# Optimization experiments

Hardware: AMD Instinct MI355X
Metric: run time of the kernel (lower is better)

The kernel has to match this reference:

```python
import jax, jax.numpy as jnp
import numpy as np

L_DEG = 4      # max out-degree L
DEPTH = 7      # complete L-ary tree depth -> 21845 nodes
N_GEN = 16
C_ST = 8
M_LAB = 256


def _build_tree():
    sizes = [L_DEG ** d for d in range(DEPTH + 1)]
    limits = np.concatenate([[0], np.cumsum(sizes)]).astype(np.int64)
    t_size = int(limits[-1])
    nodes = np.arange(t_size)
    rng = np.random.default_rng(0)
    labels = rng.integers(0, M_LAB, t_size)
    parent = np.where(nodes > 0, (nodes - 1) // L_DEG, 0)
    pos = np.where(nodes > 0, (nodes - 1) % L_DEG, 0)
    ch = np.zeros((t_size, L_DEG), dtype=np.int64)
    n_internal = int(limits[-2])
    ch[:n_internal] = L_DEG * nodes[:n_internal, None] + np.arange(1, L_DEG + 1)[None, :]
    t = np.concatenate([labels[:, None], parent[:, None], pos[:, None], ch], axis=1).astype(np.int64)
    return t, limits


def setup_inputs() -> dict:
    key = jax.random.key(0)
    ka, kb, kp, ks = jax.random.split(key, 4)
    t, limits = _build_tree()
    return {
        "t": jnp.asarray(t),
        "t_limits": jnp.asarray(limits),
        "a": jax.random.normal(ka, (N_GEN, C_ST, C_ST, L_DEG), dtype=jnp.float32),
        "b": jax.random.normal(kb, (N_GEN, C_ST, M_LAB), dtype=jnp.float32),
        "pi": jax.random.normal(kp, (N_GEN, C_ST, L_DEG), dtype=jnp.float32),
        "sp": jax.random.normal(ks, (N_GEN, L_DEG), dtype=jnp.float32),
    }


def _forward(tn, lim, a, b, pi, sp):
    # tn, lim are host numpy int arrays (tree structure is a constant).
    G, C, _, L = a.shape
    t_size = int(lim[-1])
    n_levels = len(lim) - 1
    sL = int(lim[-2])                      # first leaf index
    labels = tn[:, 0]
    posf = tn[:, 2]
    ch_all = tn[:, 3:3 + L]

    sm_a = jax.nn.softmax(a, axis=1)       # P(parent_state i | child_state j, pos l)
    sm_b = jax.nn.softmax(b, axis=2)
    sm_pi = jax.nn.softmax(pi, axis=1)
    sm_sp = jax.nn.softmax(sp, axis=1)
    a_sp = sm_a * sm_sp[:, None, None, :]  # [G,i,j,L]

    # ---------------- upward pass ----------------
    prior = jnp.zeros((t_size, G, C), a.dtype)
    beta = jnp.zeros((t_size, G, C), a.dtype)
    beta_il = jnp.zeros((t_size, G, C), a.dtype)

    prior_lv = jnp.moveaxis(sm_pi[:, :, posf[sL:]], 2, 0)   # [NL,G,C]
    emis_lv = jnp.moveaxis(sm_b[:, :, labels[sL:]], 2, 0)   # [NL,G,C]
    beta_lv = prior_lv * emis_lv
    beta_lv = beta_lv / jnp.sum(beta_lv, axis=2, keepdims=True)
    prior = prior.at[sL:].set(prior_lv)
    beta = beta.at[sL:].set(beta_lv)

    for lev in range(n_levels - 2, -1, -1):   # internal levels, bottom-up
        s, e = int(lim[lev]), int(lim[lev + 1])
        ch = ch_all[s:e]                       # [P,L]
        mask = (ch > 0).astype(a.dtype)        # children packed in first slots
        prior_ch = prior[ch]                   # [P,L,G,C]
        beta_ch = beta[ch]                     # [P,L,G,C]
        u_prior = jnp.einsum('gijl,pl,plgj->pgi', a_sp, mask, prior_ch)
        u_bil = jnp.einsum('gijl,pl,plgj->pgi', a_sp, mask, beta_ch) / u_prior
        emis = jnp.moveaxis(sm_b[:, :, labels[s:e]], 2, 0)  # [P,G,C]
        tmp = emis * u_bil * u_prior
        u_beta = tmp / jnp.sum(tmp, axis=2, keepdims=True)
        prior = prior.at[s:e].set(u_prior)
        beta = beta.at[s:e].set(u_beta)
        beta_il = beta_il.at[s:e].set(u_bil)

    # ---------------- downward pass ----------------
    # row t_size is a dummy slot for padded (absent) children
    eps_i = jnp.zeros((t_size + 1, G, C), a.dtype).at[0].set(beta[0])
    eps_ijl = jnp.zeros((t_size, G, C, C, L), a.dtype)
    for lev in range(0, n_levels - 1):         # parents, top-down (root included)
        s, e = int(lim[lev]), int(lim[lev + 1])
        ch = ch_all[s:e]
        maskb = ch > 0
        mask = maskb.astype(a.dtype)
        beta_ch = jnp.transpose(beta[ch], (0, 2, 3, 1))       # [P,G,Cj,L]
        pe = eps_i[s:e] / (prior[s:e] * beta_il[s:e])         # [P,G,Ci]
        res = (pe[:, :, :, None, None] * a_sp[None]
               * beta_ch[:, :, None, :, :]
               * mask[:, None, None, None, :])                # [P,G,i,j,L]
        child_eps = jnp.sum(res, axis=3)                       # sum over j (as in source) -> [P,G,i,L]
        vals = jnp.moveaxis(child_eps, 3, 1).reshape(-1, G, C) # [P*L,G,C]
        safe = np.where(maskb, ch, t_size).reshape(-1)
        eps_i = eps_i.at[safe].set(vals)
        eps_ijl = eps_ijl.at[s:e].set(res)
    eps_i = eps_i[:t_size]
    # leaves' eps_ijl stay zero (source scatters zeros there)

    # ---------------- log-likelihood ----------------
    a_lh = jnp.einsum('ugijl,gijl->g', eps_ijl, jnp.log(sm_a))
    b_lh = jnp.einsum('ugc,gcu->g', eps_i, jnp.log(sm_b)[:, :, labels])
    pi_lh = jnp.einsum('ugc,gcu->g', eps_i[sL:], jnp.log(sm_pi)[:, :, posf[sL:]])
    eps_l = jnp.sum(eps_ijl, axis=(2, 3))                      # [u,g,L]
    sp_lh = jnp.einsum('ugl,gl->g', eps_l, jnp.log(sm_sp))
    return a_lh + b_lh + pi_lh + sp_lh


def reference(t, t_limits, a, b, pi, sp):
    tn = np.asarray(t)
    lim = np.asarray(t_limits)
    return _forward(tn, lim, a, b, pi, sp)
```

## Files before the change

### kernel.cpp

```cpp
#include <hip/hip_runtime.h>


#define G 16
#define C 8
#define GC 128
#define TSIZE 21845
#define SL 5461

__device__ __forceinline__ float grp8_sum(float v) {
  v += __shfl_xor(v, 1);
  v += __shfl_xor(v, 2);
  v += __shfl_xor(v, 4);
  return v;
}

__global__ void setup_kernel(const float* __restrict__ ain, const float* __restrict__ bin,
                             const float* __restrict__ piin, const float* __restrict__ spin,
                             float* __restrict__ a_sp, float* __restrict__ log_a,
                             float* __restrict__ sm_bT, float* __restrict__ log_bT,
                             float* __restrict__ sm_piT, float* __restrict__ log_piT,
                             float* __restrict__ log_sp, float* __restrict__ out) {
  int blk = blockIdx.x, tid = threadIdx.x;
  if (blk < 16) {
    int g = blk;
    __shared__ float red4[4];
    for (int c = 0; c < 8; ++c) {
      int row = g * 8 + c;
      float x = bin[row * 256 + tid];
      float m = x;
      #pragma unroll
      for (int off2 = 32; off2; off2 >>= 1) m = fmaxf(m, __shfl_xor(m, off2));
      if ((tid & 63) == 0) red4[tid >> 6] = m;
      __syncthreads();
      m = fmaxf(fmaxf(red4[0], red4[1]), fmaxf(red4[2], red4[3]));
      __syncthreads();
      float e = expf(x - m);
      float ssum = e;
      #pragma unroll
      for (int off2 = 32; off2; off2 >>= 1) ssum += __shfl_xor(ssum, off2);
      if ((tid & 63) == 0) red4[tid >> 6] = ssum;
      __syncthreads();
      ssum = red4[0] + red4[1] + red4[2] + red4[3];
      __syncthreads();
      sm_bT[tid * GC + row]  = e / ssum;
      log_bT[tid * GC + row] = (x - m) - logf(ssum);
    }
  } else if (blk == 16) {
    for (int col = tid; col < 512; col += 256) {
      int g = col >> 5, j = (col >> 2) & 7, l = col & 3;
      float x[8], m = -1e30f;
      #pragma unroll
      for (int i = 0; i < 8; ++i) { x[i] = ain[g*256 + i*32 + j*4 + l]; m = fmaxf(m, x[i]); }
      float ssum = 0.f;
      #pragma unroll
      for (int i = 0; i < 8; ++i) ssum += expf(x[i] - m);
      float ls = logf(ssum);
      float y0 = spin[g*4+0], y1 = spin[g*4+1], y2 = spin[g*4+2], y3 = spin[g*4+3];
      float ms = fmaxf(fmaxf(y0, y1), fmaxf(y2, y3));
      float d = expf(y0-ms) + expf(y1-ms) + expf(y2-ms) + expf(y3-ms);
      float spv = expf(spin[g*4+l] - ms) / d;
      #pragma unroll
      for (int i = 0; i < 8; ++i) {
        int o2 = g*256 + i*32 + j*4 + l;
        float smv = expf(x[i] - m) / ssum;
        a_sp[o2]  = smv * spv;
        log_a[o2] = (x[i] - m) - ls;
      }
    }
  } else {
    if (tid < 64) {
      int g = tid >> 2, l = tid & 3;
      float x[8], m = -1e30f;
      #pragma unroll
      for (int c = 0; c < 8; ++c) { x[c] = piin[g*32 + c*4 + l]; m = fmaxf(m, x[c]); }
      float ssum = 0.f;
      #pragma unroll
      for (int c = 0; c < 8; ++c) ssum += expf(x[c] - m);
      float ls = logf(ssum);
      #pragma unroll
      for (int c = 0; c < 8; ++c) {
        sm_piT[l*GC + g*8 + c]  = expf(x[c] - m) / ssum;
        log_piT[l*GC + g*8 + c] = (x[c] - m) - ls;
      }
    } else if (tid < 80) {
      int g = tid - 64;
      float y[4], m = -1e30f;
      #pragma unroll
      for (int l = 0; l < 4; ++l) { y[l] = spin[g*4 + l]; m = fmaxf(m, y[l]); }
      float ssum = 0.f;
      #pragma unroll
      for (int l = 0; l < 4; ++l) ssum += expf(y[l] - m);
      float ls = logf(ssum);
      #pragma unroll
      for (int l = 0; l < 4; ++l) log_sp[g*4 + l] = (y[l] - m) - ls;
    } else if (tid >= 128 && tid < 144) {
      out[tid - 128] = 0.0f;
    }
  }
}

__device__ __forceinline__ void up_step(int u, int gi, const float* asp,
    const float* __restrict__ sm_bT, const int* __restrict__ t,
    float* __restrict__ beta, float* __restrict__ numbeta) {
  int ch0 = 4*u + 1;
  int g8 = gi & 0x78;
  float ub = 0.f;
  #pragma unroll
  for (int l = 0; l < 4; ++l) {
    const float4* bp = (const float4*)(beta + (size_t)(ch0 + l) * GC + g8);
    float4 b0 = bp[0], b1 = bp[1];
    ub += asp[l]*b0.x + asp[4+l]*b0.y + asp[8+l]*b0.z + asp[12+l]*b0.w
        + asp[16+l]*b1.x + asp[20+l]*b1.y + asp[24+l]*b1.z + asp[28+l]*b1.w;
  }
  float tmp = sm_bT[t[u*7] * GC + gi] * ub;
  float s = grp8_sum(tmp);
  size_t o = (size_t)u * GC + gi;
  beta[o]    = tmp / s;
  numbeta[o] = ub;
}

__device__ __forceinline__ double down_step(int u, int gi, const float* asp,
    const float* aal, const float* lsp,
    const float* __restrict__ log_bT, const int* __restrict__ t,
    const float* __restrict__ numbeta, const float* __restrict__ beta,
    float* __restrict__ eps) {
  size_t o = (size_t)u * GC + gi;
  float e  = eps[o];
  float pe = e / numbeta[o];
  int ch0 = 4*u + 1;
  int g8 = gi & 0x78;
  float local = 0.f;
  #pragma unroll
  for (int l = 0; l < 4; ++l) {
    const float4* bp = (const float4*)(beta + (size_t)(ch0 + l) * GC + g8);
    float4 b0 = bp[0], b1 = bp[1];
    float S = asp[l]*b0.x + asp[4+l]*b0.y + asp[8+l]*b0.z + asp[12+l]*b0.w
            + asp[16+l]*b1.x + asp[20+l]*b1.y + asp[24+l]*b1.z + asp[28+l]*b1.w;
    float A = aal[l]*b0.x + aal[4+l]*b0.y + aal[8+l]*b0.z + aal[12+l]*b0.w
            + aal[16+l]*b1.x + aal[20+l]*b1.y + aal[24+l]*b1.z + aal[28+l]*b1.w;
    float ce = pe * S;
    eps[(size_t)(ch0 + l) * GC + gi] = ce;
    local += pe*A + ce*lsp[l];
  }
  return (double)local + (double)(e * log_bT[t[u*7] * GC + gi]);
}

__global__ __launch_bounds__(512, 2) void up_kernel(
    const float* __restrict__ a_sp, const float* __restrict__ sm_bT,
    const float* __restrict__ sm_piT, const int* __restrict__ t,
    float* __restrict__ beta, float* __restrict__ numbeta) {
  int b = blockIdx.x, tid = threadIdx.x;
  int gi = tid & 127;
  float asp[32];
  {
    const float4* pa = (const float4*)(a_sp + (gi >> 3)*256 + (gi & 7)*32);
    #pragma unroll
    for (int q = 0; q < 8; ++q) {
      float4 v = pa[q];
      asp[q*4+0]=v.x; asp[q*4+1]=v.y; asp[q*4+2]=v.z; asp[q*4+3]=v.w;
    }
  }
  for (int it = 0; it < 16; ++it) {
    int k = it*4 + (tid >> 7);
    int u = SL + b*64 + k;
    float bt = sm_piT[(k & 3) * GC + gi] * sm_bT[t[u*7] * GC + gi];
    float s = grp8_sum(bt);
    beta[(size_t)u * GC + gi] = bt / s;
  }
  __syncthreads();
  for (int it = 0; it < 4; ++it)
    up_step(1365 + b*16 + it*4 + (tid >> 7), gi, asp, sm_bT, t, beta, numbeta);
  __syncthreads();
  up_step(341 + b*4 + (tid >> 7), gi, asp, sm_bT, t, beta, numbeta);
  __syncthreads();
  if (tid < 128) up_step(85 + b, gi, asp, sm_bT, t, beta, numbeta);
}

__global__ __launch_bounds__(512, 2) void top_kernel(
    const float* __restrict__ a_sp, const float* __restrict__ log_a,
    const float* __restrict__ log_sp, const float* __restrict__ sm_bT,
    const float* __restrict__ log_bT, const int* __restrict__ t,
    float* __restrict__ beta, float* __restrict__ numbeta,
    float* __restrict__ eps, float* __restrict__ out) {
  int g = blockIdx.x, tid = threadIdx.x;
  int i = tid & 7, gi = g*8 + i, q = tid >> 3;
  float asp[32], aal[32], lsp[4];
  {
    const float4* pa = (const float4*)(a_sp + g*256 + i*32);
    const float4* pl = (const float4*)(log_a + g*256 + i*32);
    #pragma unroll
    for (int k = 0; k < 8; ++k) {
      float4 va = pa[k], vl = pl[k];
      asp[k*4+0]=va.x; asp[k*4+1]=va.y; asp[k*4+2]=va.z; asp[k*4+3]=va.w;
      aal[k*4+0]=va.x*vl.x; aal[k*4+1]=va.y*vl.y; aal[k*4+2]=va.z*vl.z; aal[k*4+3]=va.w*vl.w;
    }
    #pragma unroll
    for (int l = 0; l < 4; ++l) lsp[l] = log_sp[g*4 + l];
  }
  up_step(21 + q, gi, asp, sm_bT, t, beta, numbeta);
  __syncthreads();
  if (tid < 128) up_step(5 + q, gi, asp, sm_bT, t, beta, numbeta);
  __syncthreads();
  if (tid < 32)  up_step(1 + q, gi, asp, sm_bT, t, beta, numbeta);
  __syncthreads();
  if (tid < 8) {
    up_step(0, gi, asp, sm_bT, t, beta, numbeta);
    eps[gi] = beta[gi];
  }
  __syncthreads();
  double acc = 0.0;
  if (tid < 8)   acc += down_step(0, gi, asp, aal, lsp, log_bT, t, numbeta, beta, eps);
  __syncthreads();
  if (tid < 32)  acc += down_step(1 + q, gi, asp, aal, lsp, log_bT, t, numbeta, beta, eps);
  __syncthreads();
  if (tid < 128) acc += down_step(5 + q, gi, asp, aal, lsp, log_bT, t, numbeta, beta, eps);
  __syncthreads();
  acc += down_step(21 + q, gi, asp, aal, lsp, log_bT, t, numbeta, beta, eps);
  acc += __shfl_xor(acc, 1);
  acc += __shfl_xor(acc, 2);
  acc += __shfl_xor(acc, 4);
  __shared__ double sd[64];
  if (i == 0) sd[tid >> 3] = acc;
  __syncthreads();
  if (tid == 0) {
    double s = 0.0;
    for (int k = 0; k < 64; ++k) s += sd[k];
    atomicAdd(&out[g], (float)s);
  }
}

__global__ __launch_bounds__(512, 2) void down_kernel(
    const float* __restrict__ a_sp, const float* __restrict__ log_a,
    const float* __restrict__ log_sp, const float* __restrict__ log_bT,
    const float* __restrict__ log_piT, const int* __restrict__ t,
    const float* __restrict__ numbeta, const float* __restrict__ beta,
    float* __restrict__ eps, float* __restrict__ out) {
  int b = blockIdx.x, tid = threadIdx.x;
  int gi = tid & 127, g = gi >> 3, i = gi & 7;
  float asp[32], aal[32], lsp[4];
  {
    const float4* pa = (const float4*)(a_sp + g*256 + i*32);
    const float4* pl = (const float4*)(log_a + g*256 + i*32);
    #pragma unroll
    for (int k = 0; k < 8; ++k) {
      float4 va = pa[k], vl = pl[k];
      asp[k*4+0]=va.x; asp[k*4+1]=va.y; asp[k*4+2]=va.z; asp[k*4+3]=va.w;
      aal[k*4+0]=va.x*vl.x; aal[k*4+1]=va.y*vl.y; aal[k*4+2]=va.z*vl.z; aal[k*4+3]=va.w*vl.w;
    }
    #pragma unroll
    for (int l = 0; l < 4; ++l) lsp[l] = log_sp[g*4 + l];
  }
  double acc = 0.0;
  if (tid < 128)
    acc += down_step(85 + b, gi, asp, aal, lsp, log_bT, t, numbeta, beta, eps);
  __syncthreads();
  acc += down_step(341 + b*4 + (tid >> 7), gi, asp, aal, lsp, log_bT, t, numbeta, beta, eps);
  __syncthreads();
  for (int it = 0; it < 4; ++it)
    acc += down_step(1365 + b*16 + it*4 + (tid >> 7), gi, asp, aal, lsp, log_bT, t,
                     numbeta, beta, eps);
  __syncthreads();
  for (int it = 0; it < 16; ++it) {
    int k = it*4 + (tid >> 7);
    int u = SL + b*64 + k;
    float e = eps[(size_t)u * GC + gi];
    acc += (double)(e * (log_bT[t[u*7] * GC + gi] + log_piT[(k & 3) * GC + gi]));
  }
  acc += __shfl_xor(acc, 1);
  acc += __shfl_xor(acc, 2);
  acc += __shfl_xor(acc, 4);
  __shared__ double sd[64];
  if (i == 0) sd[(tid >> 7)*16 + g] = acc;
  __syncthreads();
  if (tid < 16) {
    double s = sd[tid] + sd[16 + tid] + sd[32 + tid] + sd[48 + tid];
    atomicAdd(&out[tid], (float)s);
  }
}

extern "C" void kernel_launch(void* const* d_in, const int* in_sizes, int n_in,
                              void* d_out, int out_size, void* d_ws, size_t ws_size,
                              hipStream_t stream) {
  const int*   t  = (const int*)d_in[0];
  const float* a  = (const float*)d_in[2];
  const float* b  = (const float*)d_in[3];
  const float* pi = (const float*)d_in[4];
  const float* sp = (const float*)d_in[5];
  float* out = (float*)d_out;

  char* w = (char*)d_ws;
  size_t off = 0;
  auto carve = [&](size_t bytes) -> void* {
    void* p = w + off;
    off += (bytes + 255) & ~(size_t)255;
    return p;
  };
  float* a_sp    = (float*)carve((size_t)16*8*8*4*4);
  float* log_a   = (float*)carve((size_t)16*8*8*4*4);
  float* sm_bT   = (float*)carve((size_t)256*GC*4);
  float* log_bT  = (float*)carve((size_t)256*GC*4);
  float* sm_piT  = (float*)carve((size_t)4*GC*4);
  float* log_piT = (float*)carve((size_t)4*GC*4);
  float* log_sp  = (float*)carve((size_t)16*4*4);
  float* beta    = (float*)carve((size_t)TSIZE*GC*4);
  float* numbeta = (float*)carve((size_t)SL*GC*4);
  float* eps     = (float*)carve((size_t)TSIZE*GC*4);

  setup_kernel<<<18, 256, 0, stream>>>(a, b, pi, sp, a_sp, log_a, sm_bT, log_bT,
                                       sm_piT, log_piT, log_sp, out);
  up_kernel<<<256, 512, 0, stream>>>(a_sp, sm_bT, sm_piT, t, beta, numbeta);
  top_kernel<<<16, 512, 0, stream>>>(a_sp, log_a, log_sp, sm_bT, log_bT, t,
                                     beta, numbeta, eps, out);
  down_kernel<<<256, 512, 0, stream>>>(a_sp, log_a, log_sp, log_bT, log_piT, t,
                                       numbeta, beta, eps, out);
}
```

Before: 122.3 us.

## Fuse setup, upward, top and downward passes into one cooperative kernel with LDS subtrees

Merges the four launches into a single cooperative kernel separated by grid-wide syncs. Each block keeps its 85-node subtree's beta, numbeta and eps in shared memory instead of global buffers, so only the top 341 nodes go through global memory. This removes launch gaps and most global traffic for the large per-node arrays. In exchange it adds grid-sync cost, lowers occupancy to one block per CU, and leaves most of the grid idle while 16 blocks handle the top of the tree.

```diff
diff --git a/kernel.cpp b/kernel.cpp
--- a/kernel.cpp
+++ b/kernel.cpp
@@ -1,4 +1,7 @@
 #include <hip/hip_runtime.h>
+#include <hip/hip_cooperative_groups.h>
+
+namespace cg = cooperative_groups;
 
 
 #define G 16
@@ -7,6 +10,14 @@
 #define TSIZE 21845
 #define SL 5461
 
+struct P {
+  const int* t;
+  const float* a; const float* b; const float* pi; const float* sp;
+  float* a_sp; float* log_a; float* sm_bT; float* log_bT;
+  float* sm_piT; float* log_piT; float* log_sp;
+  float* betaG; float* numG; float* epsG; float* out;
+};
+
 __device__ __forceinline__ float grp8_sum(float v) {
   v += __shfl_xor(v, 1);
   v += __shfl_xor(v, 2);
@@ -14,303 +25,331 @@
   return v;
 }
 
-__global__ void setup_kernel(const float* __restrict__ ain, const float* __restrict__ bin,
-                             const float* __restrict__ piin, const float* __restrict__ spin,
-                             float* __restrict__ a_sp, float* __restrict__ log_a,
-                             float* __restrict__ sm_bT, float* __restrict__ log_bT,
-                             float* __restrict__ sm_piT, float* __restrict__ log_piT,
-                             float* __restrict__ log_sp, float* __restrict__ out) {
-  int blk = blockIdx.x, tid = threadIdx.x;
-  if (blk < 16) {
-    int g = blk;
-    __shared__ float red4[4];
-    for (int c = 0; c < 8; ++c) {
-      int row = g * 8 + c;
-      float x = bin[row * 256 + tid];
-      float m = x;
-      #pragma unroll
-      for (int off2 = 32; off2; off2 >>= 1) m = fmaxf(m, __shfl_xor(m, off2));
-      if ((tid & 63) == 0) red4[tid >> 6] = m;
-      __syncthreads();
-      m = fmaxf(fmaxf(red4[0], red4[1]), fmaxf(red4[2], red4[3]));
-      __syncthreads();
-      float e = expf(x - m);
-      float ssum = e;
-      #pragma unroll
-      for (int off2 = 32; off2; off2 >>= 1) ssum += __shfl_xor(ssum, off2);
-      if ((tid & 63) == 0) red4[tid >> 6] = ssum;
-      __syncthreads();
-      ssum = red4[0] + red4[1] + red4[2] + red4[3];
-      __syncthreads();
-      sm_bT[tid * GC + row]  = e / ssum;
-      log_bT[tid * GC + row] = (x - m) - logf(ssum);
-    }
-  } else if (blk == 16) {
-    for (int col = tid; col < 512; col += 256) {
-      int g = col >> 5, j = (col >> 2) & 7, l = col & 3;
-      float x[8], m = -1e30f;
-      #pragma unroll
-      for (int i = 0; i < 8; ++i) { x[i] = ain[g*256 + i*32 + j*4 + l]; m = fmaxf(m, x[i]); }
-      float ssum = 0.f;
-      #pragma unroll
-      for (int i = 0; i < 8; ++i) ssum += expf(x[i] - m);
-      float ls = logf(ssum);
-      float y0 = spin[g*4+0], y1 = spin[g*4+1], y2 = spin[g*4+2], y3 = spin[g*4+3];
-      float ms = fmaxf(fmaxf(y0, y1), fmaxf(y2, y3));
-      float d = expf(y0-ms) + expf(y1-ms) + expf(y2-ms) + expf(y3-ms);
-      float spv = expf(spin[g*4+l] - ms) / d;
-      #pragma unroll
-      for (int i = 0; i < 8; ++i) {
-        int o2 = g*256 + i*32 + j*4 + l;
-        float smv = expf(x[i] - m) / ssum;
-        a_sp[o2]  = smv * spv;
-        log_a[o2] = (x[i] - m) - ls;
-      }
-    }
-  } else {
-    if (tid < 64) {
-      int g = tid >> 2, l = tid & 3;
-      float x[8], m = -1e30f;
-      #pragma unroll
-      for (int c = 0; c < 8; ++c) { x[c] = piin[g*32 + c*4 + l]; m = fmaxf(m, x[c]); }
-      float ssum = 0.f;
-      #pragma unroll
-      for (int c = 0; c < 8; ++c) ssum += expf(x[c] - m);
-      float ls = logf(ssum);
-      #pragma unroll
-      for (int c = 0; c < 8; ++c) {
-        sm_piT[l*GC + g*8 + c]  = expf(x[c] - m) / ssum;
-        log_piT[l*GC + g*8 + c] = (x[c] - m) - ls;
-      }
-    } else if (tid < 80) {
-      int g = tid - 64;
-      float y[4], m = -1e30f;
-      #pragma unroll
-      for (int l = 0; l < 4; ++l) { y[l] = spin[g*4 + l]; m = fmaxf(m, y[l]); }
-      float ssum = 0.f;
-      #pragma unroll
-      for (int l = 0; l < 4; ++l) ssum += expf(y[l] - m);
-      float ls = logf(ssum);
-      #pragma unroll
-      for (int l = 0; l < 4; ++l) log_sp[g*4 + l] = (y[l] - m) - ls;
-    } else if (tid >= 128 && tid < 144) {
-      out[tid - 128] = 0.0f;
-    }
-  }
-}
-
-__device__ __forceinline__ void up_step(int u, int gi, const float* asp,
-    const float* __restrict__ sm_bT, const int* __restrict__ t,
-    float* __restrict__ beta, float* __restrict__ numbeta) {
-  int ch0 = 4*u + 1;
-  int g8 = gi & 0x78;
+__device__ __forceinline__ void up_lds(int v, int lab, int gi, int g8,
+    const float* asp, const float* __restrict__ sm_bT,
+    float* sBeta, float* sNum) {
+  int ch0 = 4*v + 1;
   float ub = 0.f;
   #pragma unroll
   for (int l = 0; l < 4; ++l) {
-    const float4* bp = (const float4*)(beta + (size_t)(ch0 + l) * GC + g8);
+    const float4* bp = (const float4*)(sBeta + (ch0 + l)*GC + g8);
     float4 b0 = bp[0], b1 = bp[1];
     ub += asp[l]*b0.x + asp[4+l]*b0.y + asp[8+l]*b0.z + asp[12+l]*b0.w
         + asp[16+l]*b1.x + asp[20+l]*b1.y + asp[24+l]*b1.z + asp[28+l]*b1.w;
   }
-  float tmp = sm_bT[t[u*7] * GC + gi] * ub;
+  float tmp = sm_bT[lab*GC + gi] * ub;
   float s = grp8_sum(tmp);
-  size_t o = (size_t)u * GC + gi;
-  beta[o]    = tmp / s;
-  numbeta[o] = ub;
-}
-
-__device__ __forceinline__ double down_step(int u, int gi, const float* asp,
-    const float* aal, const float* lsp,
-    const float* __restrict__ log_bT, const int* __restrict__ t,
-    const float* __restrict__ numbeta, const float* __restrict__ beta,
-    float* __restrict__ eps) {
-  size_t o = (size_t)u * GC + gi;
-  float e  = eps[o];
-  float pe = e / numbeta[o];
-  int ch0 = 4*u + 1;
-  int g8 = gi & 0x78;
+  sBeta[v*GC + gi] = tmp / s;
+  sNum[v*GC + gi]  = ub;
+}
+
+__device__ __forceinline__ double down_lds(int v, int lab, float e, int gi, int g8,
+    const float* asp, const float* aal, const float* lsp,
+    const float* __restrict__ log_bT, float* sBeta, const float* sNum) {
+  float pe = e / sNum[v*GC + gi];
+  int ch0 = 4*v + 1;
   float local = 0.f;
   #pragma unroll
   for (int l = 0; l < 4; ++l) {
-    const float4* bp = (const float4*)(beta + (size_t)(ch0 + l) * GC + g8);
+    float4* bp = (float4*)(sBeta + (ch0 + l)*GC + g8);
     float4 b0 = bp[0], b1 = bp[1];
     float S = asp[l]*b0.x + asp[4+l]*b0.y + asp[8+l]*b0.z + asp[12+l]*b0.w
             + asp[16+l]*b1.x + asp[20+l]*b1.y + asp[24+l]*b1.z + asp[28+l]*b1.w;
     float A = aal[l]*b0.x + aal[4+l]*b0.y + aal[8+l]*b0.z + aal[12+l]*b0.w
             + aal[16+l]*b1.x + aal[20+l]*b1.y + aal[24+l]*b1.z + aal[28+l]*b1.w;
     float ce = pe * S;
-    eps[(size_t)(ch0 + l) * GC + gi] = ce;
+    sBeta[(ch0 + l)*GC + gi] = ce;
     local += pe*A + ce*lsp[l];
   }
-  return (double)local + (double)(e * log_bT[t[u*7] * GC + gi]);
-}
-
-__global__ __launch_bounds__(512, 2) void up_kernel(
-    const float* __restrict__ a_sp, const float* __restrict__ sm_bT,
-    const float* __restrict__ sm_piT, const int* __restrict__ t,
-    float* __restrict__ beta, float* __restrict__ numbeta) {
-  int b = blockIdx.x, tid = threadIdx.x;
-  int gi = tid & 127;
+  return (double)local + (double)(e * log_bT[lab*GC + gi]);
+}
+
+__device__ __forceinline__ void up_g(int u, int lab, int gi, int g8,
+    const float* asp, const float* __restrict__ sm_bT,
+    float* __restrict__ betaG, float* __restrict__ numG) {
+  int ch0 = 4*u + 1;
+  float ub = 0.f;
+  #pragma unroll
+  for (int l = 0; l < 4; ++l) {
+    const float4* bp = (const float4*)(betaG + (size_t)(ch0 + l)*GC + g8);
+    float4 b0 = bp[0], b1 = bp[1];
+    ub += asp[l]*b0.x + asp[4+l]*b0.y + asp[8+l]*b0.z + asp[12+l]*b0.w
+        + asp[16+l]*b1.x + asp[20+l]*b1.y + asp[24+l]*b1.z + asp[28+l]*b1.w;
+  }
+  float tmp = sm_bT[lab*GC + gi] * ub;
+  float s = grp8_sum(tmp);
+  betaG[(size_t)u*GC + gi] = tmp / s;
+  numG[(size_t)u*GC + gi]  = ub;
+}
+
+__device__ __forceinline__ double down_g(int u, int lab, int gi, int g8,
+    const float* asp, const float* aal, const float* lsp,
+    const float* __restrict__ log_bT, const float* __restrict__ numG,
+    const float* __restrict__ betaG, float* __restrict__ epsG) {
+  float e  = epsG[(size_t)u*GC + gi];
+  float pe = e / numG[(size_t)u*GC + gi];
+  int ch0 = 4*u + 1;
+  float local = 0.f;
+  #pragma unroll
+  for (int l = 0; l < 4; ++l) {
+    const float4* bp = (const float4*)(betaG + (size_t)(ch0 + l)*GC + g8);
+    float4 b0 = bp[0], b1 = bp[1];
+    float S = asp[l]*b0.x + asp[4+l]*b0.y + asp[8+l]*b0.z + asp[12+l]*b0.w
+            + asp[16+l]*b1.x + asp[20+l]*b1.y + asp[24+l]*b1.z + asp[28+l]*b1.w;
+    float A = aal[l]*b0.x + aal[4+l]*b0.y + aal[8+l]*b0.z + aal[12+l]*b0.w
+            + aal[16+l]*b1.x + aal[20+l]*b1.y + aal[24+l]*b1.z + aal[28+l]*b1.w;
+    float ce = pe * S;
+    epsG[(size_t)(ch0 + l)*GC + gi] = ce;
+    local += pe*A + ce*lsp[l];
+  }
+  return (double)local + (double)(e * log_bT[lab*GC + gi]);
+}
+
+__global__ __launch_bounds__(512, 1) void fused_kernel(P p) {
+  __shared__ float  sBeta[85*GC];
+  __shared__ float  sNum[21*GC];
+  __shared__ double sd[64];
+  __shared__ float  red[2][4];
+  cg::grid_group grid = cg::this_grid();
+  const int blk = blockIdx.x, tid = threadIdx.x;
+
+  if (blk < 16) {
+    int g = blk, lab = tid & 255, half = tid >> 8;
+    #pragma unroll
+    for (int cc = 0; cc < 4; ++cc) {
+      int c = half*4 + cc, row = g*8 + c;
+      float x = p.b[row*256 + lab];
+      float m = x;
+      #pragma unroll
+      for (int o2 = 32; o2; o2 >>= 1) m = fmaxf(m, __shfl_xor(m, o2));
+      if ((tid & 63) == 0) red[half][(tid >> 6) & 3] = m;
+      __syncthreads();
+      m = fmaxf(fmaxf(red[half][0], red[half][1]), fmaxf(red[half][2], red[half][3]));
+      __syncthreads();
+      float e = expf(x - m);
+      float s = e;
+      #pragma unroll
+      for (int o2 = 32; o2; o2 >>= 1) s += __shfl_xor(s, o2);
+      if ((tid & 63) == 0) red[half][(tid >> 6) & 3] = s;
+      __syncthreads();
+      s = red[half][0] + red[half][1] + red[half][2] + red[half][3];
+      __syncthreads();
+      p.sm_bT[lab*GC + row]  = e / s;
+      p.log_bT[lab*GC + row] = (x - m) - logf(s);
+    }
+  } else if (blk == 16) {
+    int col = tid;
+    int g = col >> 5, j = (col >> 2) & 7, l = col & 3;
+    float x[8], m = -1e30f;
+    #pragma unroll
+    for (int i = 0; i < 8; ++i) { x[i] = p.a[g*256 + i*32 + j*4 + l]; m = fmaxf(m, x[i]); }
+    float ssum = 0.f;
+    #pragma unroll
+    for (int i = 0; i < 8; ++i) ssum += expf(x[i] - m);
+    float ls = logf(ssum);
+    float y0 = p.sp[g*4+0], y1 = p.sp[g*4+1], y2 = p.sp[g*4+2], y3 = p.sp[g*4+3];
+    float ms = fmaxf(fmaxf(y0, y1), fmaxf(y2, y3));
+    float d = expf(y0-ms) + expf(y1-ms) + expf(y2-ms) + expf(y3-ms);
+    float spv = expf(p.sp[g*4+l] - ms) / d;
+    #pragma unroll
+    for (int i = 0; i < 8; ++i) {
+      int o2 = g*256 + i*32 + j*4 + l;
+      p.a_sp[o2]  = expf(x[i] - m) / ssum * spv;
+      p.log_a[o2] = (x[i] - m) - ls;
+    }
+  } else if (blk == 17) {
+    if (tid < 64) {
+      int g = tid >> 2, l = tid & 3;
+      float x[8], m = -1e30f;
+      #pragma unroll
+      for (int c = 0; c < 8; ++c) { x[c] = p.pi[g*32 + c*4 + l]; m = fmaxf(m, x[c]); }
+      float ssum = 0.f;
+      #pragma unroll
+      for (int c = 0; c < 8; ++c) ssum += expf(x[c] - m);
+      float ls = logf(ssum);
+      #pragma unroll
+      for (int c = 0; c < 8; ++c) {
+        p.sm_piT[l*GC + g*8 + c]  = expf(x[c] - m) / ssum;
+        p.log_piT[l*GC + g*8 + c] = (x[c] - m) - ls;
+      }
+    } else if (tid < 80) {
+      int g = tid - 64;
+      float y[4], m = -1e30f;
+      #pragma unroll
+      for (int l = 0; l < 4; ++l) { y[l] = p.sp[g*4 + l]; m = fmaxf(m, y[l]); }
+      float ssum = 0.f;
+      #pragma unroll
+      for (int l = 0; l < 4; ++l) ssum += expf(y[l] - m);
+      float ls = logf(ssum);
+      #pragma unroll
+      for (int l = 0; l < 4; ++l) p.log_sp[g*4 + l] = (y[l] - m) - ls;
+    } else if (tid >= 128 && tid < 144) {
+      p.out[tid - 128] = 0.0f;
+    }
+  }
+  grid.sync();
+
+  const int gi = tid & 127, g = gi >> 3, i = gi & 7, g8 = g*8;
   float asp[32];
   {
-    const float4* pa = (const float4*)(a_sp + (gi >> 3)*256 + (gi & 7)*32);
+    const float4* pa = (const float4*)(p.a_sp + g*256 + i*32);
     #pragma unroll
     for (int q = 0; q < 8; ++q) {
       float4 v = pa[q];
       asp[q*4+0]=v.x; asp[q*4+1]=v.y; asp[q*4+2]=v.z; asp[q*4+3]=v.w;
     }
   }
+  const int base_leaf = SL + blk*64;
   for (int it = 0; it < 16; ++it) {
     int k = it*4 + (tid >> 7);
-    int u = SL + b*64 + k;
-    float bt = sm_piT[(k & 3) * GC + gi] * sm_bT[t[u*7] * GC + gi];
+    float bt = p.sm_piT[(k & 3)*GC + gi] * p.sm_bT[p.t[(base_leaf + k)*7]*GC + gi];
     float s = grp8_sum(bt);
-    beta[(size_t)u * GC + gi] = bt / s;
-  }
-  __syncthreads();
-  for (int it = 0; it < 4; ++it)
-    up_step(1365 + b*16 + it*4 + (tid >> 7), gi, asp, sm_bT, t, beta, numbeta);
-  __syncthreads();
-  up_step(341 + b*4 + (tid >> 7), gi, asp, sm_bT, t, beta, numbeta);
-  __syncthreads();
-  if (tid < 128) up_step(85 + b, gi, asp, sm_bT, t, beta, numbeta);
-}
-
-__global__ __launch_bounds__(512, 2) void top_kernel(
-    const float* __restrict__ a_sp, const float* __restrict__ log_a,
-    const float* __restrict__ log_sp, const float* __restrict__ sm_bT,
-    const float* __restrict__ log_bT, const int* __restrict__ t,
-    float* __restrict__ beta, float* __restrict__ numbeta,
-    float* __restrict__ eps, float* __restrict__ out) {
-  int g = blockIdx.x, tid = threadIdx.x;
-  int i = tid & 7, gi = g*8 + i, q = tid >> 3;
-  float asp[32], aal[32], lsp[4];
+    sBeta[(21 + k)*GC + gi] = bt / s;
+  }
+  __syncthreads();
+  for (int it = 0; it < 4; ++it) {
+    int k = it*4 + (tid >> 7);
+    up_lds(5 + k, p.t[(1365 + blk*16 + k)*7], gi, g8, asp, p.sm_bT, sBeta, sNum);
+  }
+  __syncthreads();
   {
-    const float4* pa = (const float4*)(a_sp + g*256 + i*32);
-    const float4* pl = (const float4*)(log_a + g*256 + i*32);
+    int k = tid >> 7;
+    up_lds(1 + k, p.t[(341 + blk*4 + k)*7], gi, g8, asp, p.sm_bT, sBeta, sNum);
+  }
+  __syncthreads();
+  if (tid < 128) {
+    up_lds(0, p.t[(85 + blk)*7], gi, g8, asp, p.sm_bT, sBeta, sNum);
+    p.betaG[(size_t)(85 + blk)*GC + gi] = sBeta[gi];
+  }
+  grid.sync();
+
+  if (blk < 16) {
+    int it_ = tid & 7, q = tid >> 3, gt = blk*8 + it_, g8t = blk*8;
+    float aspt[32], aalt[32], lspt[4];
+    {
+      const float4* pa = (const float4*)(p.a_sp  + blk*256 + it_*32);
+      const float4* pl = (const float4*)(p.log_a + blk*256 + it_*32);
+      #pragma unroll
+      for (int k = 0; k < 8; ++k) {
+        float4 va = pa[k], vl = pl[k];
+        aspt[k*4+0]=va.x; aspt[k*4+1]=va.y; aspt[k*4+2]=va.z; aspt[k*4+3]=va.w;
+        aalt[k*4+0]=va.x*vl.x; aalt[k*4+1]=va.y*vl.y; aalt[k*4+2]=va.z*vl.z; aalt[k*4+3]=va.w*vl.w;
+      }
+      #pragma unroll
+      for (int l = 0; l < 4; ++l) lspt[l] = p.log_sp[blk*4 + l];
+    }
+    up_g(21 + q, p.t[(21 + q)*7], gt, g8t, aspt, p.sm_bT, p.betaG, p.numG);
+    __syncthreads();
+    if (tid < 128) up_g(5 + q, p.t[(5 + q)*7], gt, g8t, aspt, p.sm_bT, p.betaG, p.numG);
+    __syncthreads();
+    if (tid < 32)  up_g(1 + q, p.t[(1 + q)*7], gt, g8t, aspt, p.sm_bT, p.betaG, p.numG);
+    __syncthreads();
+    if (tid < 8) {
+      up_g(0, p.t[0], gt, g8t, aspt, p.sm_bT, p.betaG, p.numG);
+      p.epsG[gt] = p.betaG[gt];
+    }
+    __syncthreads();
+    double acc = 0.0;
+    if (tid < 8)
+      acc += down_g(0, p.t[0], gt, g8t, aspt, aalt, lspt, p.log_bT, p.numG, p.betaG, p.epsG);
+    __syncthreads();
+    if (tid < 32)
+      acc += down_g(1 + q, p.t[(1 + q)*7], gt, g8t, aspt, aalt, lspt, p.log_bT, p.numG, p.betaG, p.epsG);
+    __syncthreads();
+    if (tid < 128)
+      acc += down_g(5 + q, p.t[(5 + q)*7], gt, g8t, aspt, aalt, lspt, p.log_bT, p.numG, p.betaG, p.epsG);
+    __syncthreads();
+    acc += down_g(21 + q, p.t[(21 + q)*7], gt, g8t, aspt, aalt, lspt, p.log_bT, p.numG, p.betaG, p.epsG);
+    acc += __shfl_xor(acc, 1);
+    acc += __shfl_xor(acc, 2);
+    acc += __shfl_xor(acc, 4);
+    if (it_ == 0) sd[q] = acc;
+    __syncthreads();
+    if (tid == 0) {
+      double s = 0.0;
+      for (int k = 0; k < 64; ++k) s += sd[k];
+      atomicAdd(&p.out[blk], (float)s);
+    }
+    __syncthreads();
+  }
+  grid.sync();
+
+  float aal[32], lsp[4];
+  {
+    const float4* pa = (const float4*)(p.a_sp  + g*256 + i*32);
+    const float4* pl = (const float4*)(p.log_a + g*256 + i*32);
     #pragma unroll
     for (int k = 0; k < 8; ++k) {
       float4 va = pa[k], vl = pl[k];
-      asp[k*4+0]=va.x; asp[k*4+1]=va.y; asp[k*4+2]=va.z; asp[k*4+3]=va.w;
       aal[k*4+0]=va.x*vl.x; aal[k*4+1]=va.y*vl.y; aal[k*4+2]=va.z*vl.z; aal[k*4+3]=va.w*vl.w;
     }
     #pragma unroll
-    for (int l = 0; l < 4; ++l) lsp[l] = log_sp[g*4 + l];
-  }
-  up_step(21 + q, gi, asp, sm_bT, t, beta, numbeta);
-  __syncthreads();
-  if (tid < 128) up_step(5 + q, gi, asp, sm_bT, t, beta, numbeta);
-  __syncthreads();
-  if (tid < 32)  up_step(1 + q, gi, asp, sm_bT, t, beta, numbeta);
-  __syncthreads();
-  if (tid < 8) {
-    up_step(0, gi, asp, sm_bT, t, beta, numbeta);
-    eps[gi] = beta[gi];
-  }
-  __syncthreads();
+    for (int l = 0; l < 4; ++l) lsp[l] = p.log_sp[g*4 + l];
+  }
   double acc = 0.0;
-  if (tid < 8)   acc += down_step(0, gi, asp, aal, lsp, log_bT, t, numbeta, beta, eps);
-  __syncthreads();
-  if (tid < 32)  acc += down_step(1 + q, gi, asp, aal, lsp, log_bT, t, numbeta, beta, eps);
-  __syncthreads();
-  if (tid < 128) acc += down_step(5 + q, gi, asp, aal, lsp, log_bT, t, numbeta, beta, eps);
-  __syncthreads();
-  acc += down_step(21 + q, gi, asp, aal, lsp, log_bT, t, numbeta, beta, eps);
+  if (tid < 128) {
+    float e = p.epsG[(size_t)(85 + blk)*GC + gi];
+    acc += down_lds(0, p.t[(85 + blk)*7], e, gi, g8, asp, aal, lsp, p.log_bT, sBeta, sNum);
+  }
+  __syncthreads();
+  {
+    int k = tid >> 7, v = 1 + k;
+    float e = sBeta[v*GC + gi];
+    acc += down_lds(v, p.t[(341 + blk*4 + k)*7], e, gi, g8, asp, aal, lsp, p.log_bT, sBeta, sNum);
+  }
+  __syncthreads();
+  for (int it = 0; it < 4; ++it) {
+    int k = it*4 + (tid >> 7), v = 5 + k;
+    float e = sBeta[v*GC + gi];
+    acc += down_lds(v, p.t[(1365 + blk*16 + k)*7], e, gi, g8, asp, aal, lsp, p.log_bT, sBeta, sNum);
+  }
+  __syncthreads();
+  for (int it = 0; it < 16; ++it) {
+    int k = it*4 + (tid >> 7);
+    float e = sBeta[(21 + k)*GC + gi];
+    acc += (double)(e * (p.log_bT[p.t[(base_leaf + k)*7]*GC + gi] +
+                         p.log_piT[(k & 3)*GC + gi]));
+  }
   acc += __shfl_xor(acc, 1);
   acc += __shfl_xor(acc, 2);
   acc += __shfl_xor(acc, 4);
-  __shared__ double sd[64];
   if (i == 0) sd[tid >> 3] = acc;
-  __syncthreads();
-  if (tid == 0) {
-    double s = 0.0;
-    for (int k = 0; k < 64; ++k) s += sd[k];
-    atomicAdd(&out[g], (float)s);
-  }
-}
-
-__global__ __launch_bounds__(512, 2) void down_kernel(
-    const float* __restrict__ a_sp, const float* __restrict__ log_a,
-    const float* __restrict__ log_sp, const float* __restrict__ log_bT,
-    const float* __restrict__ log_piT, const int* __restrict__ t,
-    const float* __restrict__ numbeta, const float* __restrict__ beta,
-    float* __restrict__ eps, float* __restrict__ out) {
-  int b = blockIdx.x, tid = threadIdx.x;
-  int gi = tid & 127, g = gi >> 3, i = gi & 7;
-  float asp[32], aal[32], lsp[4];
-  {
-    const float4* pa = (const float4*)(a_sp + g*256 + i*32);
-    const float4* pl = (const float4*)(log_a + g*256 + i*32);
-    #pragma unroll
-    for (int k = 0; k < 8; ++k) {
-      float4 va = pa[k], vl = pl[k];
-      asp[k*4+0]=va.x; asp[k*4+1]=va.y; asp[k*4+2]=va.z; asp[k*4+3]=va.w;
-      aal[k*4+0]=va.x*vl.x; aal[k*4+1]=va.y*vl.y; aal[k*4+2]=va.z*vl.z; aal[k*4+3]=va.w*vl.w;
-    }
-    #pragma unroll
-    for (int l = 0; l < 4; ++l) lsp[l] = log_sp[g*4 + l];
-  }
-  double acc = 0.0;
-  if (tid < 128)
-    acc += down_step(85 + b, gi, asp, aal, lsp, log_bT, t, numbeta, beta, eps);
-  __syncthreads();
-  acc += down_step(341 + b*4 + (tid >> 7), gi, asp, aal, lsp, log_bT, t, numbeta, beta, eps);
-  __syncthreads();
-  for (int it = 0; it < 4; ++it)
-    acc += down_step(1365 + b*16 + it*4 + (tid >> 7), gi, asp, aal, lsp, log_bT, t,
-                     numbeta, beta, eps);
-  __syncthreads();
-  for (int it = 0; it < 16; ++it) {
-    int k = it*4 + (tid >> 7);
-    int u = SL + b*64 + k;
-    float e = eps[(size_t)u * GC + gi];
-    acc += (double)(e * (log_bT[t[u*7] * GC + gi] + log_piT[(k & 3) * GC + gi]));
-  }
-  acc += __shfl_xor(acc, 1);
-  acc += __shfl_xor(acc, 2);
-  acc += __shfl_xor(acc, 4);
-  __shared__ double sd[64];
-  if (i == 0) sd[(tid >> 7)*16 + g] = acc;
   __syncthreads();
   if (tid < 16) {
     double s = sd[tid] + sd[16 + tid] + sd[32 + tid] + sd[48 + tid];
-    atomicAdd(&out[tid], (float)s);
+    atomicAdd(&p.out[tid], (float)s);
   }
 }
 
 extern "C" void kernel_launch(void* const* d_in, const int* in_sizes, int n_in,
                               void* d_out, int out_size, void* d_ws, size_t ws_size,
                               hipStream_t stream) {
-  const int*   t  = (const int*)d_in[0];
-  const float* a  = (const float*)d_in[2];
-  const float* b  = (const float*)d_in[3];
-  const float* pi = (const float*)d_in[4];
-  const float* sp = (const float*)d_in[5];
-  float* out = (float*)d_out;
-
   char* w = (char*)d_ws;
   size_t off = 0;
   auto carve = [&](size_t bytes) -> void* {
-    void* p = w + off;
+    void* ptr = w + off;
     off += (bytes + 255) & ~(size_t)255;
-    return p;
+    return ptr;
   };
-  float* a_sp    = (float*)carve((size_t)16*8*8*4*4);
-  float* log_a   = (float*)carve((size_t)16*8*8*4*4);
-  float* sm_bT   = (float*)carve((size_t)256*GC*4);
-  float* log_bT  = (float*)carve((size_t)256*GC*4);
-  float* sm_piT  = (float*)carve((size_t)4*GC*4);
-  float* log_piT = (float*)carve((size_t)4*GC*4);
-  float* log_sp  = (float*)carve((size_t)16*4*4);
-  float* beta    = (float*)carve((size_t)TSIZE*GC*4);
-  float* numbeta = (float*)carve((size_t)SL*GC*4);
-  float* eps     = (float*)carve((size_t)TSIZE*GC*4);
-
-  setup_kernel<<<18, 256, 0, stream>>>(a, b, pi, sp, a_sp, log_a, sm_bT, log_bT,
-                                       sm_piT, log_piT, log_sp, out);
-  up_kernel<<<256, 512, 0, stream>>>(a_sp, sm_bT, sm_piT, t, beta, numbeta);
-  top_kernel<<<16, 512, 0, stream>>>(a_sp, log_a, log_sp, sm_bT, log_bT, t,
-                                     beta, numbeta, eps, out);
-  down_kernel<<<256, 512, 0, stream>>>(a_sp, log_a, log_sp, log_bT, log_piT, t,
-                                       numbeta, beta, eps, out);
-}
+  P p;
+  p.t  = (const int*)d_in[0];
+  p.a  = (const float*)d_in[2];
+  p.b  = (const float*)d_in[3];
+  p.pi = (const float*)d_in[4];
+  p.sp = (const float*)d_in[5];
+  p.a_sp    = (float*)carve((size_t)16*8*8*4*4);
+  p.log_a   = (float*)carve((size_t)16*8*8*4*4);
+  p.sm_bT   = (float*)carve((size_t)256*GC*4);
+  p.log_bT  = (float*)carve((size_t)256*GC*4);
+  p.sm_piT  = (float*)carve((size_t)4*GC*4);
+  p.log_piT = (float*)carve((size_t)4*GC*4);
+  p.log_sp  = (float*)carve((size_t)16*4*4);
+  p.betaG   = (float*)carve((size_t)341*GC*4);
+  p.numG    = (float*)carve((size_t)85*GC*4);
+  p.epsG    = (float*)carve((size_t)341*GC*4);
+  p.out     = (float*)d_out;
+
+  void* args[] = { &p };
+  hipLaunchCooperativeKernel((const void*)fused_kernel, dim3(256), dim3(512),
+                             args, 0, stream);
+}
```

Measured after the change: 187.3 us. 1.53x slower.

## Keep per-subtree beta/eps in LDS and recompute upward pass in down kernel

Applied to the files above, without the earlier changes.

Each block's 85-node subtree (levels 4-7) now lives in shared memory, so the up kernel writes only the subtree root's beta to global memory. The down kernel recomputes the subtree's upward beta and numbeta in LDS rather than reading the large global beta, numbeta and eps arrays. eps values overwrite beta in place inside LDS. Blocks grow to 1024 threads, and the global workspace shrinks to the top 341 nodes. This trades duplicated upward compute and a larger LDS footprint, with lower occupancy, for removing megabytes of global round-trip traffic.

```diff
diff --git a/kernel.cpp b/kernel.cpp
--- a/kernel.cpp
+++ b/kernel.cpp
@@ -99,91 +99,134 @@
   }
 }
 
-__device__ __forceinline__ void up_step(int u, int gi, const float* asp,
-    const float* __restrict__ sm_bT, const int* __restrict__ t,
-    float* __restrict__ beta, float* __restrict__ numbeta) {
-  int ch0 = 4*u + 1;
-  int g8 = gi & 0x78;
+__device__ __forceinline__ void up_lds(int v, int lab, int gi, int g8,
+    const float* asp, const float* __restrict__ sm_bT,
+    float* sBeta, float* sNum, bool wantNum) {
+  int ch0 = 4*v + 1;
   float ub = 0.f;
   #pragma unroll
   for (int l = 0; l < 4; ++l) {
-    const float4* bp = (const float4*)(beta + (size_t)(ch0 + l) * GC + g8);
+    const float4* bp = (const float4*)(sBeta + (ch0 + l)*GC + g8);
     float4 b0 = bp[0], b1 = bp[1];
     ub += asp[l]*b0.x + asp[4+l]*b0.y + asp[8+l]*b0.z + asp[12+l]*b0.w
         + asp[16+l]*b1.x + asp[20+l]*b1.y + asp[24+l]*b1.z + asp[28+l]*b1.w;
   }
-  float tmp = sm_bT[t[u*7] * GC + gi] * ub;
+  float tmp = sm_bT[lab*GC + gi] * ub;
   float s = grp8_sum(tmp);
-  size_t o = (size_t)u * GC + gi;
-  beta[o]    = tmp / s;
-  numbeta[o] = ub;
-}
-
-__device__ __forceinline__ double down_step(int u, int gi, const float* asp,
-    const float* aal, const float* lsp,
-    const float* __restrict__ log_bT, const int* __restrict__ t,
-    const float* __restrict__ numbeta, const float* __restrict__ beta,
-    float* __restrict__ eps) {
-  size_t o = (size_t)u * GC + gi;
-  float e  = eps[o];
-  float pe = e / numbeta[o];
-  int ch0 = 4*u + 1;
-  int g8 = gi & 0x78;
+  sBeta[v*GC + gi] = tmp / s;
+  if (wantNum) sNum[v*GC + gi] = ub;
+}
+
+__device__ __forceinline__ double down_lds(int v, int lab, float e, int gi, int g8,
+    const float* asp, const float* aal, const float* lsp,
+    const float* __restrict__ log_bT, float* sBeta, const float* sNum) {
+  float pe = e / sNum[v*GC + gi];
+  int ch0 = 4*v + 1;
   float local = 0.f;
   #pragma unroll
   for (int l = 0; l < 4; ++l) {
-    const float4* bp = (const float4*)(beta + (size_t)(ch0 + l) * GC + g8);
+    float4* bp = (float4*)(sBeta + (ch0 + l)*GC + g8);
     float4 b0 = bp[0], b1 = bp[1];
     float S = asp[l]*b0.x + asp[4+l]*b0.y + asp[8+l]*b0.z + asp[12+l]*b0.w
             + asp[16+l]*b1.x + asp[20+l]*b1.y + asp[24+l]*b1.z + asp[28+l]*b1.w;
     float A = aal[l]*b0.x + aal[4+l]*b0.y + aal[8+l]*b0.z + aal[12+l]*b0.w
             + aal[16+l]*b1.x + aal[20+l]*b1.y + aal[24+l]*b1.z + aal[28+l]*b1.w;
     float ce = pe * S;
-    eps[(size_t)(ch0 + l) * GC + gi] = ce;
+    sBeta[(ch0 + l)*GC + gi] = ce;
     local += pe*A + ce*lsp[l];
   }
-  return (double)local + (double)(e * log_bT[t[u*7] * GC + gi]);
-}
-
-__global__ __launch_bounds__(512, 2) void up_kernel(
+  return (double)local + (double)(e * log_bT[lab*GC + gi]);
+}
+
+__device__ __forceinline__ void up_g(int u, int lab, int gi, int g8,
+    const float* asp, const float* __restrict__ sm_bT,
+    float* __restrict__ betaG, float* __restrict__ numG) {
+  int ch0 = 4*u + 1;
+  float ub = 0.f;
+  #pragma unroll
+  for (int l = 0; l < 4; ++l) {
+    const float4* bp = (const float4*)(betaG + (size_t)(ch0 + l)*GC + g8);
+    float4 b0 = bp[0], b1 = bp[1];
+    ub += asp[l]*b0.x + asp[4+l]*b0.y + asp[8+l]*b0.z + asp[12+l]*b0.w
+        + asp[16+l]*b1.x + asp[20+l]*b1.y + asp[24+l]*b1.z + asp[28+l]*b1.w;
+  }
+  float tmp = sm_bT[lab*GC + gi] * ub;
+  float s = grp8_sum(tmp);
+  betaG[(size_t)u*GC + gi] = tmp / s;
+  numG[(size_t)u*GC + gi]  = ub;
+}
+
+__device__ __forceinline__ double down_g(int u, int lab, int gi, int g8,
+    const float* asp, const float* aal, const float* lsp,
+    const float* __restrict__ log_bT, const float* __restrict__ numG,
+    const float* __restrict__ betaG, float* __restrict__ epsG) {
+  float e  = epsG[(size_t)u*GC + gi];
+  float pe = e / numG[(size_t)u*GC + gi];
+  int ch0 = 4*u + 1;
+  float local = 0.f;
+  #pragma unroll
+  for (int l = 0; l < 4; ++l) {
+    const float4* bp = (const float4*)(betaG + (size_t)(ch0 + l)*GC + g8);
+    float4 b0 = bp[0], b1 = bp[1];
+    float S = asp[l]*b0.x + asp[4+l]*b0.y + asp[8+l]*b0.z + asp[12+l]*b0.w
+            + asp[16+l]*b1.x + asp[20+l]*b1.y + asp[24+l]*b1.z + asp[28+l]*b1.w;
+    float A = aal[l]*b0.x + aal[4+l]*b0.y + aal[8+l]*b0.z + aal[12+l]*b0.w
+            + aal[16+l]*b1.x + aal[20+l]*b1.y + aal[24+l]*b1.z + aal[28+l]*b1.w;
+    float ce = pe * S;
+    epsG[(size_t)(ch0 + l)*GC + gi] = ce;
+    local += pe*A + ce*lsp[l];
+  }
+  return (double)local + (double)(e * log_bT[lab*GC + gi]);
+}
+
+__global__ __launch_bounds__(1024, 1) void up_kernel(
     const float* __restrict__ a_sp, const float* __restrict__ sm_bT,
     const float* __restrict__ sm_piT, const int* __restrict__ t,
-    float* __restrict__ beta, float* __restrict__ numbeta) {
-  int b = blockIdx.x, tid = threadIdx.x;
-  int gi = tid & 127;
+    float* __restrict__ betaG) {
+  __shared__ float sBeta[85*GC];
+  const int blk = blockIdx.x, tid = threadIdx.x;
+  const int gi = tid & 127, g = gi >> 3, i = gi & 7, g8 = g*8, w = tid >> 7;
   float asp[32];
   {
-    const float4* pa = (const float4*)(a_sp + (gi >> 3)*256 + (gi & 7)*32);
+    const float4* pa = (const float4*)(a_sp + g*256 + i*32);
     #pragma unroll
     for (int q = 0; q < 8; ++q) {
       float4 v = pa[q];
       asp[q*4+0]=v.x; asp[q*4+1]=v.y; asp[q*4+2]=v.z; asp[q*4+3]=v.w;
     }
   }
-  for (int it = 0; it < 16; ++it) {
-    int k = it*4 + (tid >> 7);
-    int u = SL + b*64 + k;
-    float bt = sm_piT[(k & 3) * GC + gi] * sm_bT[t[u*7] * GC + gi];
+  const int base_leaf = SL + blk*64;
+  #pragma unroll
+  for (int it = 0; it < 8; ++it) {
+    int k = it*8 + w;
+    float bt = sm_piT[(k & 3)*GC + gi] * sm_bT[t[(base_leaf + k)*7]*GC + gi];
     float s = grp8_sum(bt);
-    beta[(size_t)u * GC + gi] = bt / s;
-  }
-  __syncthreads();
-  for (int it = 0; it < 4; ++it)
-    up_step(1365 + b*16 + it*4 + (tid >> 7), gi, asp, sm_bT, t, beta, numbeta);
-  __syncthreads();
-  up_step(341 + b*4 + (tid >> 7), gi, asp, sm_bT, t, beta, numbeta);
-  __syncthreads();
-  if (tid < 128) up_step(85 + b, gi, asp, sm_bT, t, beta, numbeta);
+    sBeta[(21 + k)*GC + gi] = bt / s;
+  }
+  __syncthreads();
+  #pragma unroll
+  for (int it = 0; it < 2; ++it) {
+    int k = it*8 + w;
+    up_lds(5 + k, t[(1365 + blk*16 + k)*7], gi, g8, asp, sm_bT, sBeta, nullptr, false);
+  }
+  __syncthreads();
+  if (tid < 512)
+    up_lds(1 + w, t[(341 + blk*4 + w)*7], gi, g8, asp, sm_bT, sBeta, nullptr, false);
+  __syncthreads();
+  if (tid < 128) {
+    up_lds(0, t[(85 + blk)*7], gi, g8, asp, sm_bT, sBeta, nullptr, false);
+    betaG[(size_t)(85 + blk)*GC + gi] = sBeta[gi];
+  }
 }
 
 __global__ __launch_bounds__(512, 2) void top_kernel(
     const float* __restrict__ a_sp, const float* __restrict__ log_a,
     const float* __restrict__ log_sp, const float* __restrict__ sm_bT,
     const float* __restrict__ log_bT, const int* __restrict__ t,
-    float* __restrict__ beta, float* __restrict__ numbeta,
-    float* __restrict__ eps, float* __restrict__ out) {
+    float* __restrict__ betaG, float* __restrict__ numG,
+    float* __restrict__ epsG, float* __restrict__ out) {
   int g = blockIdx.x, tid = threadIdx.x;
-  int i = tid & 7, gi = g*8 + i, q = tid >> 3;
+  int i = tid & 7, gi = g*8 + i, q = tid >> 3, g8 = g*8;
   float asp[32], aal[32], lsp[4];
   {
     const float4* pa = (const float4*)(a_sp + g*256 + i*32);
@@ -197,30 +240,33 @@
     #pragma unroll
     for (int l = 0; l < 4; ++l) lsp[l] = log_sp[g*4 + l];
   }
-  up_step(21 + q, gi, asp, sm_bT, t, beta, numbeta);
-  __syncthreads();
-  if (tid < 128) up_step(5 + q, gi, asp, sm_bT, t, beta, numbeta);
-  __syncthreads();
-  if (tid < 32)  up_step(1 + q, gi, asp, sm_bT, t, beta, numbeta);
+  up_g(21 + q, t[(21 + q)*7], gi, g8, asp, sm_bT, betaG, numG);
+  __syncthreads();
+  if (tid < 128) up_g(5 + q, t[(5 + q)*7], gi, g8, asp, sm_bT, betaG, numG);
+  __syncthreads();
+  if (tid < 32)  up_g(1 + q, t[(1 + q)*7], gi, g8, asp, sm_bT, betaG, numG);
   __syncthreads();
   if (tid < 8) {
-    up_step(0, gi, asp, sm_bT, t, beta, numbeta);
-    eps[gi] = beta[gi];
+    up_g(0, t[0], gi, g8, asp, sm_bT, betaG, numG);
+    epsG[gi] = betaG[gi];
   }
   __syncthreads();
   double acc = 0.0;
-  if (tid < 8)   acc += down_step(0, gi, asp, aal, lsp, log_bT, t, numbeta, beta, eps);
-  __syncthreads();
-  if (tid < 32)  acc += down_step(1 + q, gi, asp, aal, lsp, log_bT, t, numbeta, beta, eps);
-  __syncthreads();
-  if (tid < 128) acc += down_step(5 + q, gi, asp, aal, lsp, log_bT, t, numbeta, beta, eps);
-  __syncthreads();
-  acc += down_step(21 + q, gi, asp, aal, lsp, log_bT, t, numbeta, beta, eps);
+  if (tid < 8)
+    acc += down_g(0, t[0], gi, g8, asp, aal, lsp, log_bT, numG, betaG, epsG);
+  __syncthreads();
+  if (tid < 32)
+    acc += down_g(1 + q, t[(1 + q)*7], gi, g8, asp, aal, lsp, log_bT, numG, betaG, epsG);
+  __syncthreads();
+  if (tid < 128)
+    acc += down_g(5 + q, t[(5 + q)*7], gi, g8, asp, aal, lsp, log_bT, numG, betaG, epsG);
+  __syncthreads();
+  acc += down_g(21 + q, t[(21 + q)*7], gi, g8, asp, aal, lsp, log_bT, numG, betaG, epsG);
   acc += __shfl_xor(acc, 1);
   acc += __shfl_xor(acc, 2);
   acc += __shfl_xor(acc, 4);
   __shared__ double sd[64];
-  if (i == 0) sd[tid >> 3] = acc;
+  if (i == 0) sd[q] = acc;
   __syncthreads();
   if (tid == 0) {
     double s = 0.0;
@@ -229,17 +275,20 @@
   }
 }
 
-__global__ __launch_bounds__(512, 2) void down_kernel(
+__global__ __launch_bounds__(1024, 1) void down_kernel(
     const float* __restrict__ a_sp, const float* __restrict__ log_a,
-    const float* __restrict__ log_sp, const float* __restrict__ log_bT,
+    const float* __restrict__ log_sp, const float* __restrict__ sm_bT,
+    const float* __restrict__ log_bT, const float* __restrict__ sm_piT,
     const float* __restrict__ log_piT, const int* __restrict__ t,
-    const float* __restrict__ numbeta, const float* __restrict__ beta,
-    float* __restrict__ eps, float* __restrict__ out) {
-  int b = blockIdx.x, tid = threadIdx.x;
-  int gi = tid & 127, g = gi >> 3, i = gi & 7;
+    const float* __restrict__ epsG, float* __restrict__ out) {
+  __shared__ float  sBeta[85*GC];
+  __shared__ float  sNum[21*GC];
+  __shared__ double sd[128];
+  const int blk = blockIdx.x, tid = threadIdx.x;
+  const int gi = tid & 127, g = gi >> 3, i = gi & 7, g8 = g*8, w = tid >> 7;
   float asp[32], aal[32], lsp[4];
   {
-    const float4* pa = (const float4*)(a_sp + g*256 + i*32);
+    const float4* pa = (const float4*)(a_sp  + g*256 + i*32);
     const float4* pl = (const float4*)(log_a + g*256 + i*32);
     #pragma unroll
     for (int k = 0; k < 8; ++k) {
@@ -250,30 +299,60 @@
     #pragma unroll
     for (int l = 0; l < 4; ++l) lsp[l] = log_sp[g*4 + l];
   }
+  const int base_leaf = SL + blk*64;
+  #pragma unroll
+  for (int it = 0; it < 8; ++it) {
+    int k = it*8 + w;
+    float bt = sm_piT[(k & 3)*GC + gi] * sm_bT[t[(base_leaf + k)*7]*GC + gi];
+    float s = grp8_sum(bt);
+    sBeta[(21 + k)*GC + gi] = bt / s;
+  }
+  __syncthreads();
+  #pragma unroll
+  for (int it = 0; it < 2; ++it) {
+    int k = it*8 + w;
+    up_lds(5 + k, t[(1365 + blk*16 + k)*7], gi, g8, asp, sm_bT, sBeta, sNum, true);
+  }
+  __syncthreads();
+  if (tid < 512)
+    up_lds(1 + w, t[(341 + blk*4 + w)*7], gi, g8, asp, sm_bT, sBeta, sNum, true);
+  __syncthreads();
   double acc = 0.0;
-  if (tid < 128)
-    acc += down_step(85 + b, gi, asp, aal, lsp, log_bT, t, numbeta, beta, eps);
-  __syncthreads();
-  acc += down_step(341 + b*4 + (tid >> 7), gi, asp, aal, lsp, log_bT, t, numbeta, beta, eps);
-  __syncthreads();
-  for (int it = 0; it < 4; ++it)
-    acc += down_step(1365 + b*16 + it*4 + (tid >> 7), gi, asp, aal, lsp, log_bT, t,
-                     numbeta, beta, eps);
-  __syncthreads();
-  for (int it = 0; it < 16; ++it) {
-    int k = it*4 + (tid >> 7);
-    int u = SL + b*64 + k;
-    float e = eps[(size_t)u * GC + gi];
-    acc += (double)(e * (log_bT[t[u*7] * GC + gi] + log_piT[(k & 3) * GC + gi]));
+  if (tid < 128) {
+    up_lds(0, t[(85 + blk)*7], gi, g8, asp, sm_bT, sBeta, sNum, true);
+    float e = epsG[(size_t)(85 + blk)*GC + gi];
+    acc += down_lds(0, t[(85 + blk)*7], e, gi, g8, asp, aal, lsp, log_bT, sBeta, sNum);
+  }
+  __syncthreads();
+  if (tid < 512) {
+    int v = 1 + w;
+    float e = sBeta[v*GC + gi];
+    acc += down_lds(v, t[(341 + blk*4 + w)*7], e, gi, g8, asp, aal, lsp, log_bT, sBeta, sNum);
+  }
+  __syncthreads();
+  #pragma unroll
+  for (int it = 0; it < 2; ++it) {
+    int k = it*8 + w, v = 5 + k;
+    float e = sBeta[v*GC + gi];
+    acc += down_lds(v, t[(1365 + blk*16 + k)*7], e, gi, g8, asp, aal, lsp, log_bT, sBeta, sNum);
+  }
+  __syncthreads();
+  #pragma unroll
+  for (int it = 0; it < 8; ++it) {
+    int k = it*8 + w;
+    float e = sBeta[(21 + k)*GC + gi];
+    acc += (double)(e * (log_bT[t[(base_leaf + k)*7]*GC + gi] +
+                         log_piT[(k & 3)*GC + gi]));
   }
   acc += __shfl_xor(acc, 1);
   acc += __shfl_xor(acc, 2);
   acc += __shfl_xor(acc, 4);
-  __shared__ double sd[64];
-  if (i == 0) sd[(tid >> 7)*16 + g] = acc;
+  if (i == 0) sd[tid >> 3] = acc;
   __syncthreads();
   if (tid < 16) {
-    double s = sd[tid] + sd[16 + tid] + sd[32 + tid] + sd[48 + tid];
+    double s = 0.0;
+    #pragma unroll
+    for (int c = 0; c < 8; ++c) s += sd[tid + 16*c];
     atomicAdd(&out[tid], (float)s);
   }
 }
@@ -291,9 +370,9 @@
   char* w = (char*)d_ws;
   size_t off = 0;
   auto carve = [&](size_t bytes) -> void* {
-    void* p = w + off;
+    void* ptr = w + off;
     off += (bytes + 255) & ~(size_t)255;
-    return p;
+    return ptr;
   };
   float* a_sp    = (float*)carve((size_t)16*8*8*4*4);
   float* log_a   = (float*)carve((size_t)16*8*8*4*4);
@@ -302,15 +381,15 @@
   float* sm_piT  = (float*)carve((size_t)4*GC*4);
   float* log_piT = (float*)carve((size_t)4*GC*4);
   float* log_sp  = (float*)carve((size_t)16*4*4);
-  float* beta    = (float*)carve((size_t)TSIZE*GC*4);
-  float* numbeta = (float*)carve((size_t)SL*GC*4);
-  float* eps     = (float*)carve((size_t)TSIZE*GC*4);
+  float* betaG   = (float*)carve((size_t)341*GC*4);
+  float* numG    = (float*)carve((size_t)85*GC*4);
+  float* epsG    = (float*)carve((size_t)341*GC*4);
 
   setup_kernel<<<18, 256, 0, stream>>>(a, b, pi, sp, a_sp, log_a, sm_bT, log_bT,
                                        sm_piT, log_piT, log_sp, out);
-  up_kernel<<<256, 512, 0, stream>>>(a_sp, sm_bT, sm_piT, t, beta, numbeta);
+  up_kernel<<<256, 1024, 0, stream>>>(a_sp, sm_bT, sm_piT, t, betaG);
   top_kernel<<<16, 512, 0, stream>>>(a_sp, log_a, log_sp, sm_bT, log_bT, t,
-                                     beta, numbeta, eps, out);
-  down_kernel<<<256, 512, 0, stream>>>(a_sp, log_a, log_sp, log_bT, log_piT, t,
-                                       numbeta, beta, eps, out);
-}
+                                     betaG, numG, epsG, out);
+  down_kernel<<<256, 1024, 0, stream>>>(a_sp, log_a, log_sp, sm_bT, log_bT,
+                                        sm_piT, log_piT, t, epsG, out);
+}
```

Measured after the change: 116.6 us. -4.7%, faster.
